# Optimization experiments

Hardware: AMD Instinct MI355X
Metric: run time of the kernel (lower is better)

## Reference

```python
import jax, jax.numpy as jnp
import numpy as np

N_NODES = 50000
N_EDGES = 800000
IN_F = 128
HID = 16
HEADS = 8
OUT_F = 128


def setup_inputs() -> dict:
    key = jax.random.key(0)
    ks = jax.random.split(key, 16)
    h = jax.random.normal(ks[0], (N_NODES, IN_F), dtype=jnp.float32)
    src1 = jax.random.randint(ks[1], (N_EDGES,), 0, N_NODES, dtype=jnp.int32)
    dst1 = jax.random.randint(ks[2], (N_EDGES,), 0, N_NODES, dtype=jnp.int32)
    src2 = jax.random.randint(ks[3], (N_EDGES,), 0, N_NODES, dtype=jnp.int32)
    dst2 = jax.random.randint(ks[4], (N_EDGES,), 0, N_NODES, dtype=jnp.int32)
    norm1 = jax.random.uniform(ks[5], (N_NODES, 1), dtype=jnp.float32)
    norm2 = jax.random.uniform(ks[6], (N_NODES, 1), dtype=jnp.float32)
    D = HEADS * HID  # 128
    W_lin = jax.random.normal(ks[7], (IN_F, D), dtype=jnp.float32) * (1.0 / np.sqrt(IN_F))
    b_lin = jax.random.normal(ks[8], (D,), dtype=jnp.float32) * 0.01
    al = jax.random.normal(ks[9], (HEADS, HID, 1), dtype=jnp.float32) * 0.1
    ar = jax.random.normal(ks[10], (HEADS, HID, 1), dtype=jnp.float32) * 0.1
    W_fc = jax.random.normal(ks[11], (D, OUT_F), dtype=jnp.float32) * (1.0 / np.sqrt(D))
    b_fc = jax.random.normal(ks[12], (OUT_F,), dtype=jnp.float32) * 0.01
    return {"h": h, "src1": src1, "dst1": dst1, "src2": src2, "dst2": dst2,
            "norm1": norm1, "norm2": norm2, "W_lin": W_lin, "b_lin": b_lin,
            "al": al, "ar": ar, "W_fc": W_fc, "b_fc": b_fc}


def _propagate(feat, norm, src, dst, n_nodes):
    # msg = h[src] * norm[src]; accum[v] = sum_{e: dst=v} msg_e; out = accum * norm
    msg = feat[src] * norm[src]                      # [E, D]
    agg = jax.ops.segment_sum(msg, dst, num_segments=n_nodes)
    return agg * norm                                # [N, D]


def _leaky_relu(x):
    return jnp.where(x > 0, x, 0.2 * x)


def reference(h, src1, dst1, src2, dst2, norm1, norm2, W_lin, b_lin, al, ar, W_fc, b_fc):
    N = h.shape[0]
    hf = h @ W_lin + b_lin                           # [N, 8*HID] (dropout p given but eval-mode -> identity)
    h1 = _propagate(hf, norm1, src1, dst1, N)
    h2 = _propagate(hf, norm2, src2, dst2, N)
    # Faithful to torch: row-major reshape [N, 8*HID] -> (8, N, HID)
    h1r = h1.reshape(HEADS, N, HID)
    h2r = h2.reshape(HEADS, N, HID)
    hr = hf.reshape(HEADS, N, HID)
    ai = jnp.einsum('hnd,hdo->hno', hr, al)          # [8, N, 1]
    aj1 = jnp.einsum('hnd,hdo->hno', h1r, ar)
    aj2 = jnp.einsum('hnd,hdo->hno', h2r, ar)
    a1 = jnp.clip(jnp.exp(_leaky_relu(ai + aj1)), -10.0, 10.0)
    a2 = jnp.clip(jnp.exp(_leaky_relu(ai + aj2)), -10.0, 10.0)
    denom = a1 + a2
    out = (a1 / denom) * h1r + (a2 / denom) * h2r    # [8, N, HID]
    out = out.reshape(N, HEADS * HID)
    return out @ W_fc + b_fc
```

## Files before the change

### kernel.cpp

```cpp
#include <hip/hip_runtime.h>

#define NN 50000
#define NE 800000
#define NB 196
#define NBG 392
#define NBLK 128
#define CHUNK 6250
#define MAXB 6144

typedef __bf16 bf16x8 __attribute__((ext_vector_type(8)));
typedef float  f32x4  __attribute__((ext_vector_type(4)));

__device__ __forceinline__ unsigned short f2bf(float x) {
    unsigned u = __float_as_uint(x);
    return (unsigned short)((u + 0x7FFFu + ((u >> 16) & 1u)) >> 16);
}
__device__ __forceinline__ float bflo(unsigned u) { return __uint_as_float(u << 16); }
__device__ __forceinline__ float bfhi(unsigned u) { return __uint_as_float(u & 0xFFFF0000u); }

__global__ __launch_bounds__(1024) void histA_kernel(
    const int* __restrict__ dst1, const int* __restrict__ dst2, int* __restrict__ histG,
    const float* __restrict__ Wa, const float* __restrict__ Wb,
    unsigned short* __restrict__ Wta, unsigned short* __restrict__ Wtb)
{
    const int t = threadIdx.x, blk = blockIdx.x;
    if (blk >= NBLK) {
        const float* W = (blk - NBLK) ? Wb : Wa;
        unsigned short* Wt = (blk - NBLK) ? Wtb : Wta;
        for (int j = t; j < 128 * 128; j += 1024) {
            int n = j >> 7, k = j & 127;
            Wt[j] = f2bf(W[k * 128 + n]);
        }
        return;
    }
    __shared__ int h[NBG];
    for (int i = t; i < NBG; i += 1024) h[i] = 0;
    __syncthreads();
    const int base = blk * CHUNK;
    for (int i = t; i < CHUNK; i += 1024) {
        atomicAdd(&h[dst1[base + i] >> 8], 1);
        atomicAdd(&h[NB + (dst2[base + i] >> 8)], 1);
    }
    __syncthreads();
    for (int i = t; i < NBG; i += 1024)
        histG[blk * NBG + i] = h[i];
}

__global__ __launch_bounds__(1024) void scatterC_kernel(
    const int* __restrict__ src1, const int* __restrict__ dst1,
    const int* __restrict__ src2, const int* __restrict__ dst2,
    const int* __restrict__ histG,
    int* __restrict__ gbbase, int* __restrict__ gbtot,
    unsigned int* __restrict__ bin1, unsigned int* __restrict__ bin2)
{
    __shared__ int s[512];
    __shared__ int pos[NBG];
    const int t = threadIdx.x, blk = blockIdx.x;

    int total_i = 0, pref_i = 0;
    if (t < NBG) {
        for (int c = 0; c < NBLK; c++) {
            int v = histG[c * NBG + t];
            total_i += v;
            if (c < blk) pref_i += v;
        }
    }
    if (t < 512) s[t] = (t < NBG) ? total_i : 0;
    __syncthreads();
    for (int off = 1; off < 512; off <<= 1) {
        int x = 0;
        if (t < 512 && t >= off) x = s[t - off];
        __syncthreads();
        if (t < 512) s[t] += x;
        __syncthreads();
    }
    const int sumG1 = s[NB - 1];
    if (t < NBG) {
        int excl = s[t] - total_i;
        int bb = excl - ((t >= NB) ? sumG1 : 0);
        pos[t] = bb + pref_i;
        if (blk == 0) { gbbase[t] = bb; gbtot[t] = total_i; }
    }
    __syncthreads();

    const int base = blk * CHUNK;
    for (int i = t; i < CHUNK; i += 1024) {
        int d = dst1[base + i], sv = src1[base + i];
        int slot = atomicAdd(&pos[d >> 8], 1);
        bin1[slot] = ((unsigned)(d & 255) << 16) | (unsigned)sv;
        d = dst2[base + i]; sv = src2[base + i];
        slot = atomicAdd(&pos[NB + (d >> 8)], 1);
        bin2[slot] = ((unsigned)(d & 255) << 16) | (unsigned)sv;
    }
}

__global__ __launch_bounds__(256) void bucket_sort_kernel(
    const unsigned int* __restrict__ bin1, const unsigned int* __restrict__ bin2,
    const int* __restrict__ bbase, const int* __restrict__ btot,
    unsigned short* __restrict__ csr1, int* __restrict__ start1, int* __restrict__ deg1,
    unsigned short* __restrict__ csr2, int* __restrict__ start2, int* __restrict__ deg2)
{
    __shared__ int lcnt[256];
    __shared__ int sc[256];
    __shared__ int oat[256];
    __shared__ unsigned short outb[MAXB];
    const int t = threadIdx.x;
    const int g = (blockIdx.x >= NB) ? 1 : 0;
    const int b = blockIdx.x - g * NB;
    const unsigned int* bin = g ? bin2 : bin1;
    unsigned short* csr = g ? csr2 : csr1;
    int* start = g ? start2 : start1;
    int* deg   = g ? deg2 : deg1;

    const int base = bbase[g * NB + b];
    const int tot = min(btot[g * NB + b], MAXB);

    lcnt[t] = 0;
    __syncthreads();
    for (int i = t; i < tot; i += 256) atomicAdd(&lcnt[bin[base + i] >> 16], 1);
    __syncthreads();
    sc[t] = lcnt[t];
    __syncthreads();
    for (int off = 1; off < 256; off <<= 1) {
        int x = (t >= off) ? sc[t - off] : 0;
        __syncthreads();
        sc[t] += x;
        __syncthreads();
    }
    const int ex = sc[t] - lcnt[t];
    oat[t] = ex;
    __syncthreads();
    for (int i = t; i < tot; i += 256) {
        unsigned v = bin[base + i];
        int slot = atomicAdd(&oat[v >> 16], 1);
        outb[slot] = (unsigned short)(v & 0xFFFFu);
    }
    __syncthreads();
    for (int i = t; i < tot; i += 256) csr[base + i] = outb[i];
    int nd = b * 256 + t;
    if (nd < NN) { start[nd] = base + ex; deg[nd] = lcnt[t]; }
}

__global__ __launch_bounds__(256) void mfma_gemm_kernel(
    const float* __restrict__ X, const unsigned short* __restrict__ Wt,
    const float* __restrict__ bias, float* __restrict__ Y,
    unsigned short* __restrict__ Ybf, int nrows)
{
    __shared__ unsigned short Wl[128 * 128];
    const int t = threadIdx.x;
    const int lane = t & 63;
    const int wv = t >> 6;
    const int row0 = blockIdx.x * 64;
    const int m16 = lane & 15;
    const int quad = lane >> 4;

    {
        const uint4* Wg = (const uint4*)Wt;
        #pragma unroll
        for (int i = 0; i < 8; i++) {
            int gi = t + i * 256;
            int n = gi >> 4, g = gi & 15;
            uint4 v = Wg[gi];
            *(uint4*)&Wl[n * 128 + (((g ^ (n & 15)) << 3))] = v;
        }
    }

    const int arow = row0 + wv * 16 + m16;
    const bool valid = (arow < nrows);
    const float4* X4 = (const float4*)X;
    float4 xr[8];
    #pragma unroll
    for (int kc = 0; kc < 4; kc++) {
        if (valid) {
            int gidx = arow * 32 + kc * 8 + quad * 2;
            xr[kc * 2]     = X4[gidx];
            xr[kc * 2 + 1] = X4[gidx + 1];
        } else {
            xr[kc * 2] = xr[kc * 2 + 1] = make_float4(0.f, 0.f, 0.f, 0.f);
        }
    }
    __syncthreads();

    f32x4 acc[8];
    #pragma unroll
    for (int nt = 0; nt < 8; nt++) acc[nt] = (f32x4){0.f, 0.f, 0.f, 0.f};

    #pragma unroll
    for (int kc = 0; kc < 4; kc++) {
        union { unsigned short u[8]; bf16x8 v; } ah, al;
        float f[8] = { xr[kc*2].x, xr[kc*2].y, xr[kc*2].z, xr[kc*2].w,
                       xr[kc*2+1].x, xr[kc*2+1].y, xr[kc*2+1].z, xr[kc*2+1].w };
        #pragma unroll
        for (int j = 0; j < 8; j++) {
            unsigned u = __float_as_uint(f[j]);
            ah.u[j] = (unsigned short)(u >> 16);
            al.u[j] = f2bf(f[j] - __uint_as_float(u & 0xFFFF0000u));
        }
        const int sgbase = (kc * 4 + quad);
        #pragma unroll
        for (int nt = 0; nt < 8; nt++) {
            const int n = nt * 16 + m16;
            bf16x8 b = *(const bf16x8*)&Wl[n * 128 + ((sgbase ^ m16) << 3)];
            acc[nt] = __builtin_amdgcn_mfma_f32_16x16x32_bf16(ah.v, b, acc[nt], 0, 0, 0);
            acc[nt] = __builtin_amdgcn_mfma_f32_16x16x32_bf16(al.v, b, acc[nt], 0, 0, 0);
        }
    }

    #pragma unroll
    for (int nt = 0; nt < 8; nt++) {
        const int col = nt * 16 + m16;
        const float bc = bias[col];
        #pragma unroll
        for (int r = 0; r < 4; r++) {
            int row = row0 + wv * 16 + quad * 4 + r;
            if (row < nrows) {
                float val = acc[nt][r] + bc;
                if (Y)   Y[(long)row * 128 + col] = val;
                if (Ybf) Ybf[(long)row * 128 + col] = f2bf(val);
            }
        }
    }
}

__global__ __launch_bounds__(256) void mfma_gemm_bf16_kernel(
    const unsigned short* __restrict__ Xbf, const unsigned short* __restrict__ Wt,
    const float* __restrict__ bias, float* __restrict__ Y, int nrows)
{
    __shared__ unsigned short Wl[128 * 128];
    const int t = threadIdx.x;
    const int lane = t & 63;
    const int wv = t >> 6;
    const int row0 = blockIdx.x * 64;
    const int m16 = lane & 15;
    const int quad = lane >> 4;

    {
        const uint4* Wg = (const uint4*)Wt;
        #pragma unroll
        for (int i = 0; i < 8; i++) {
            int gi = t + i * 256;
            int n = gi >> 4, g = gi & 15;
            uint4 v = Wg[gi];
            *(uint4*)&Wl[n * 128 + (((g ^ (n & 15)) << 3))] = v;
        }
    }

    const int arow = row0 + wv * 16 + m16;
    const bool valid = (arow < nrows);
    const uint4* X16 = (const uint4*)Xbf;
    union { uint4 u; bf16x8 v; } xr[4];
    #pragma unroll
    for (int kc = 0; kc < 4; kc++) {
        if (valid) xr[kc].u = X16[arow * 16 + kc * 4 + quad];
        else       xr[kc].u = make_uint4(0, 0, 0, 0);
    }
    __syncthreads();

    f32x4 acc[8];
    #pragma unroll
    for (int nt = 0; nt < 8; nt++) acc[nt] = (f32x4){0.f, 0.f, 0.f, 0.f};

    #pragma unroll
    for (int kc = 0; kc < 4; kc++) {
        const int sgbase = (kc * 4 + quad);
        #pragma unroll
        for (int nt = 0; nt < 8; nt++) {
            const int n = nt * 16 + m16;
            bf16x8 b = *(const bf16x8*)&Wl[n * 128 + ((sgbase ^ m16) << 3)];
            acc[nt] = __builtin_amdgcn_mfma_f32_16x16x32_bf16(xr[kc].v, b, acc[nt], 0, 0, 0);
        }
    }

    #pragma unroll
    for (int nt = 0; nt < 8; nt++) {
        const int col = nt * 16 + m16;
        const float bc = bias[col];
        #pragma unroll
        for (int r = 0; r < 4; r++) {
            int row = row0 + wv * 16 + quad * 4 + r;
            if (row < nrows) Y[(long)row * 128 + col] = acc[nt][r] + bc;
        }
    }
}

__global__ __launch_bounds__(256) void gather_attn_kernel(
    const unsigned int* __restrict__ hfb,
    const unsigned short* __restrict__ csr1, const int* __restrict__ start1,
    const int* __restrict__ deg1, const float* __restrict__ norm1,
    const unsigned short* __restrict__ csr2, const int* __restrict__ start2,
    const int* __restrict__ deg2, const float* __restrict__ norm2,
    const float* __restrict__ al, const float* __restrict__ ar,
    unsigned int* __restrict__ outb)
{
    const int lane = threadIdx.x & 63;
    int node = (blockIdx.x * 256 + threadIdx.x) >> 6;
    if (node >= NN) return;
    node = __builtin_amdgcn_readfirstlane(node);

    float2 acc1 = make_float2(0.f, 0.f), acc2 = make_float2(0.f, 0.f);

    #pragma unroll 1
    for (int g = 0; g < 2; g++) {
        const unsigned short* csr = g ? csr2 : csr1;
        const int* startp = g ? start2 : start1;
        const int* degp   = g ? deg2 : deg1;
        const float* norm = g ? norm2 : norm1;
        float2 acc = make_float2(0.f, 0.f);
        const int st = startp[node], dg = degp[node];
        for (int base = 0; base < dg; base += 64) {
            const int nb = min(64, dg - base);
            int myc = (lane < nb) ? (int)csr[st + base + lane] : 0;
            int j = 0;
            for (; j + 8 <= nb; j += 8) {
                int s[8]; float n[8]; unsigned u[8];
                #pragma unroll
                for (int q = 0; q < 8; q++) s[q] = __builtin_amdgcn_readlane(myc, j + q);
                #pragma unroll
                for (int q = 0; q < 8; q++) {
                    n[q] = norm[s[q]];
                    u[q] = hfb[(long)s[q] * 64 + lane];
                }
                #pragma unroll
                for (int q = 0; q < 8; q++) {
                    acc.x = fmaf(bflo(u[q]), n[q], acc.x);
                    acc.y = fmaf(bfhi(u[q]), n[q], acc.y);
                }
            }
            for (; j < nb; j++) {
                int s = __builtin_amdgcn_readlane(myc, j);
                float nv = norm[s];
                unsigned u = hfb[(long)s * 64 + lane];
                acc.x = fmaf(bflo(u), nv, acc.x);
                acc.y = fmaf(bfhi(u), nv, acc.y);
            }
        }
        if (g) acc2 = acc; else acc1 = acc;
    }

    const float nn1 = norm1[node], nn2 = norm2[node];
    acc1.x *= nn1; acc1.y *= nn1;
    acc2.x *= nn2; acc2.y *= nn2;

    const int cc = lane >> 3;
    const int m = node * 8 + cc;
    const int head = m / NN;
    const int hid = (2 * lane) & 15;
    unsigned uf = hfb[(long)node * 64 + lane];
    const float fx = bflo(uf), fy = bfhi(uf);
    const float av0 = al[head * 16 + hid], av1 = al[head * 16 + hid + 1];
    const float rv0 = ar[head * 16 + hid], rv1 = ar[head * 16 + hid + 1];
    float s_ai = fx * av0 + fy * av1;
    float s1 = acc1.x * rv0 + acc1.y * rv1;
    float s2 = acc2.x * rv0 + acc2.y * rv1;
    s_ai += __shfl_xor(s_ai, 1); s_ai += __shfl_xor(s_ai, 2); s_ai += __shfl_xor(s_ai, 4);
    s1   += __shfl_xor(s1, 1);   s1   += __shfl_xor(s1, 2);   s1   += __shfl_xor(s1, 4);
    s2   += __shfl_xor(s2, 1);   s2   += __shfl_xor(s2, 2);   s2   += __shfl_xor(s2, 4);
    float x1 = s_ai + s1; x1 = x1 > 0.f ? x1 : 0.2f * x1;
    float x2 = s_ai + s2; x2 = x2 > 0.f ? x2 : 0.2f * x2;
    float e1 = fminf(expf(x1), 10.f);
    float e2 = fminf(expf(x2), 10.f);
    float inv = 1.f / (e1 + e2);
    float w1 = e1 * inv, w2 = e2 * inv;
    float ox = w1 * acc1.x + w2 * acc2.x;
    float oy = w1 * acc1.y + w2 * acc2.y;
    outb[(long)node * 64 + lane] = (unsigned)f2bf(ox) | ((unsigned)f2bf(oy) << 16);
}

extern "C" void kernel_launch(void* const* d_in, const int* in_sizes, int n_in,
                              void* d_out, int out_size, void* d_ws, size_t ws_size,
                              hipStream_t stream)
{
    const float* h     = (const float*)d_in[0];
    const int*   src1  = (const int*)  d_in[1];
    const int*   dst1  = (const int*)  d_in[2];
    const int*   src2  = (const int*)  d_in[3];
    const int*   dst2  = (const int*)  d_in[4];
    const float* norm1 = (const float*)d_in[5];
    const float* norm2 = (const float*)d_in[6];
    const float* W_lin = (const float*)d_in[7];
    const float* b_lin = (const float*)d_in[8];
    const float* al    = (const float*)d_in[9];
    const float* ar    = (const float*)d_in[10];
    const float* W_fc  = (const float*)d_in[11];
    const float* b_fc  = (const float*)d_in[12];
    float* out = (float*)d_out;

    unsigned short* hfb  = (unsigned short*)d_ws;
    unsigned short* outbf = hfb + (size_t)NN * 128;
    unsigned int* bin1 = (unsigned int*)(outbf + (size_t)NN * 128);
    unsigned int* bin2 = bin1 + NE;
    unsigned short* csr1 = (unsigned short*)(bin2 + NE);
    unsigned short* csr2 = csr1 + NE;
    unsigned short* WtL  = csr2 + NE;
    unsigned short* WtF  = WtL + 128 * 128;
    int* histG  = (int*)(WtF + 128 * 128);
    int* btot   = histG + NBLK * NBG;
    int* bbase  = btot + NBG;
    int* start1 = bbase + NBG;
    int* start2 = start1 + NN;
    int* deg1   = start2 + NN;
    int* deg2   = deg1 + NN;

    histA_kernel<<<NBLK + 2, 1024, 0, stream>>>(dst1, dst2, histG, W_lin, W_fc, WtL, WtF);

    mfma_gemm_kernel<<<(NN + 63) / 64, 256, 0, stream>>>(h, WtL, b_lin, nullptr, hfb, NN);

    scatterC_kernel<<<NBLK, 1024, 0, stream>>>(src1, dst1, src2, dst2, histG,
                                               bbase, btot, bin1, bin2);

    bucket_sort_kernel<<<NBG, 256, 0, stream>>>(bin1, bin2, bbase, btot,
                                                csr1, start1, deg1,
                                                csr2, start2, deg2);

    gather_attn_kernel<<<(NN * 64) / 256, 256, 0, stream>>>(
        (const unsigned int*)hfb,
        csr1, start1, deg1, norm1,
        csr2, start2, deg2, norm2,
        al, ar, (unsigned int*)outbf);

    mfma_gemm_bf16_kernel<<<(NN + 63) / 64, 256, 0, stream>>>(outbf, WtF, b_fc, out, NN);
}
```

Baseline: 229.8 us.

## Pre-scale features by norms in GEMM and batch neighbor gathers for both graphs

The first GEMM now also writes two bf16 copies of the features pre-multiplied by norm1 and norm2. This removes the per-edge norm gather and the multiply from the aggregation kernel. The gather kernel then issues up to 32 neighbor loads per graph into registers before summing, so memory parallelism is higher, and it falls back to a scalar loop for high-degree nodes. The cost is two extra N×128 bf16 writes and much higher register pressure from the 64 unrolled load slots, which may reduce occupancy. Pre-scaling also rounds the product to bf16, which changes numerics slightly.

```diff
diff --git a/kernel.cpp b/kernel.cpp
--- a/kernel.cpp
+++ b/kernel.cpp
@@ -143,8 +143,10 @@
 
 __global__ __launch_bounds__(256) void mfma_gemm_kernel(
     const float* __restrict__ X, const unsigned short* __restrict__ Wt,
-    const float* __restrict__ bias, float* __restrict__ Y,
-    unsigned short* __restrict__ Ybf, int nrows)
+    const float* __restrict__ bias,
+    const float* __restrict__ norm1, const float* __restrict__ norm2,
+    unsigned short* __restrict__ Ybf, unsigned short* __restrict__ Y1,
+    unsigned short* __restrict__ Y2, int nrows)
 {
     __shared__ unsigned short Wl[128 * 128];
     const int t = threadIdx.x;
@@ -179,6 +181,14 @@
             xr[kc * 2] = xr[kc * 2 + 1] = make_float4(0.f, 0.f, 0.f, 0.f);
         }
     }
+
+    float n1c[4], n2c[4];
+    #pragma unroll
+    for (int r = 0; r < 4; r++) {
+        int row = row0 + wv * 16 + quad * 4 + r;
+        if (row < nrows) { n1c[r] = norm1[row]; n2c[r] = norm2[row]; }
+        else             { n1c[r] = 0.f;        n2c[r] = 0.f; }
+    }
     __syncthreads();
 
     f32x4 acc[8];
@@ -215,8 +225,9 @@
             int row = row0 + wv * 16 + quad * 4 + r;
             if (row < nrows) {
                 float val = acc[nt][r] + bc;
-                if (Y)   Y[(long)row * 128 + col] = val;
-                if (Ybf) Ybf[(long)row * 128 + col] = f2bf(val);
+                Ybf[(long)row * 128 + col] = f2bf(val);
+                Y1[(long)row * 128 + col] = f2bf(val * n1c[r]);
+                Y2[(long)row * 128 + col] = f2bf(val * n2c[r]);
             }
         }
     }
@@ -285,6 +296,8 @@
 
 __global__ __launch_bounds__(256) void gather_attn_kernel(
     const unsigned int* __restrict__ hfb,
+    const unsigned int* __restrict__ hfb1,
+    const unsigned int* __restrict__ hfb2,
     const unsigned short* __restrict__ csr1, const int* __restrict__ start1,
     const int* __restrict__ deg1, const float* __restrict__ norm1,
     const unsigned short* __restrict__ csr2, const int* __restrict__ start2,
@@ -297,44 +310,51 @@
     if (node >= NN) return;
     node = __builtin_amdgcn_readfirstlane(node);
 
+    const unsigned uf = hfb[(long)node * 64 + lane];
+
+    const int st1 = start1[node], dg1 = deg1[node];
+    const int st2 = start2[node], dg2 = deg2[node];
+    const int nb1 = (dg1 < 32) ? dg1 : 32;
+    const int nb2 = (dg2 < 32) ? dg2 : 32;
+
+    int myc1 = (lane < nb1) ? (int)csr1[st1 + lane] : 0;
+    int myc2 = (lane < nb2) ? (int)csr2[st2 + lane] : 0;
+
+    unsigned uA[32], uB[32];
+    #pragma unroll
+    for (int q = 0; q < 32; q++) {
+        if (q < nb1) {
+            int s = __builtin_amdgcn_readlane(myc1, q);
+            uA[q] = hfb1[((long)s << 6) + lane];
+        }
+    }
+    #pragma unroll
+    for (int q = 0; q < 32; q++) {
+        if (q < nb2) {
+            int s = __builtin_amdgcn_readlane(myc2, q);
+            uB[q] = hfb2[((long)s << 6) + lane];
+        }
+    }
+
     float2 acc1 = make_float2(0.f, 0.f), acc2 = make_float2(0.f, 0.f);
-
-    #pragma unroll 1
-    for (int g = 0; g < 2; g++) {
-        const unsigned short* csr = g ? csr2 : csr1;
-        const int* startp = g ? start2 : start1;
-        const int* degp   = g ? deg2 : deg1;
-        const float* norm = g ? norm2 : norm1;
-        float2 acc = make_float2(0.f, 0.f);
-        const int st = startp[node], dg = degp[node];
-        for (int base = 0; base < dg; base += 64) {
-            const int nb = min(64, dg - base);
-            int myc = (lane < nb) ? (int)csr[st + base + lane] : 0;
-            int j = 0;
-            for (; j + 8 <= nb; j += 8) {
-                int s[8]; float n[8]; unsigned u[8];
-                #pragma unroll
-                for (int q = 0; q < 8; q++) s[q] = __builtin_amdgcn_readlane(myc, j + q);
-                #pragma unroll
-                for (int q = 0; q < 8; q++) {
-                    n[q] = norm[s[q]];
-                    u[q] = hfb[(long)s[q] * 64 + lane];
-                }
-                #pragma unroll
-                for (int q = 0; q < 8; q++) {
-                    acc.x = fmaf(bflo(u[q]), n[q], acc.x);
-                    acc.y = fmaf(bfhi(u[q]), n[q], acc.y);
-                }
-            }
-            for (; j < nb; j++) {
-                int s = __builtin_amdgcn_readlane(myc, j);
-                float nv = norm[s];
-                unsigned u = hfb[(long)s * 64 + lane];
-                acc.x = fmaf(bflo(u), nv, acc.x);
-                acc.y = fmaf(bfhi(u), nv, acc.y);
-            }
-        }
-        if (g) acc2 = acc; else acc1 = acc;
+    #pragma unroll
+    for (int q = 0; q < 32; q++) {
+        if (q < nb1) { acc1.x += bflo(uA[q]); acc1.y += bfhi(uA[q]); }
+    }
+    #pragma unroll
+    for (int q = 0; q < 32; q++) {
+        if (q < nb2) { acc2.x += bflo(uB[q]); acc2.y += bfhi(uB[q]); }
+    }
+
+    for (int e = 32; e < dg1; e++) {
+        int s = (int)csr1[st1 + e];
+        unsigned u = hfb1[((long)s << 6) + lane];
+        acc1.x += bflo(u); acc1.y += bfhi(u);
+    }
+    for (int e = 32; e < dg2; e++) {
+        int s = (int)csr2[st2 + e];
+        unsigned u = hfb2[((long)s << 6) + lane];
+        acc2.x += bflo(u); acc2.y += bfhi(u);
     }
 
     const float nn1 = norm1[node], nn2 = norm2[node];
@@ -345,7 +365,6 @@
     const int m = node * 8 + cc;
     const int head = m / NN;
     const int hid = (2 * lane) & 15;
-    unsigned uf = hfb[(long)node * 64 + lane];
     const float fx = bflo(uf), fy = bfhi(uf);
     const float av0 = al[head * 16 + hid], av1 = al[head * 16 + hid + 1];
     const float rv0 = ar[head * 16 + hid], rv1 = ar[head * 16 + hid + 1];
@@ -400,10 +419,13 @@
     int* start2 = start1 + NN;
     int* deg1   = start2 + NN;
     int* deg2   = deg1 + NN;
+    unsigned short* hfb1 = (unsigned short*)(deg2 + NN);
+    unsigned short* hfb2 = hfb1 + (size_t)NN * 128;
 
     histA_kernel<<<NBLK + 2, 1024, 0, stream>>>(dst1, dst2, histG, W_lin, W_fc, WtL, WtF);
 
-    mfma_gemm_kernel<<<(NN + 63) / 64, 256, 0, stream>>>(h, WtL, b_lin, nullptr, hfb, NN);
+    mfma_gemm_kernel<<<(NN + 63) / 64, 256, 0, stream>>>(h, WtL, b_lin, norm1, norm2,
+                                                         hfb, hfb1, hfb2, NN);
 
     scatterC_kernel<<<NBLK, 1024, 0, stream>>>(src1, dst1, src2, dst2, histG,
                                                bbase, btot, bin1, bin2);
@@ -413,7 +435,7 @@
                                                 csr2, start2, deg2);
 
     gather_attn_kernel<<<(NN * 64) / 256, 256, 0, stream>>>(
-        (const unsigned int*)hfb,
+        (const unsigned int*)hfb, (const unsigned int*)hfb1, (const unsigned int*)hfb2,
         csr1, start1, deg1, norm1,
         csr2, start2, deg2, norm2,
         al, ar, (unsigned int*)outbf);
```

Result: slower. 262.5 us (+14.3%).

## Issue all neighbor row loads via global_load_lds into LDS before accumulating

Applied to the files above, without the earlier changes.

The gather kernel now issues up to 32 neighbor feature-row loads per graph straight into LDS with global_load_lds, waits once, and then accumulates from LDS. Neighbor norms are loaded per lane and broadcast with readlane, and any neighbors beyond 32 fall back to a serial global loop. The goal is more memory requests in flight per wave, hiding gather latency instead of exposing it in groups of eight. In exchange it uses 32KB of LDS per 128-thread block, which may limit occupancy, and blocks shrink to two waves.

```diff
diff --git a/kernel.cpp b/kernel.cpp
--- a/kernel.cpp
+++ b/kernel.cpp
@@ -17,6 +17,15 @@
 }
 __device__ __forceinline__ float bflo(unsigned u) { return __uint_as_float(u << 16); }
 __device__ __forceinline__ float bfhi(unsigned u) { return __uint_as_float(u & 0xFFFF0000u); }
+
+__device__ __forceinline__ void gload_lds(const unsigned* g, unsigned* l) {
+    __builtin_amdgcn_global_load_lds(
+        (const __attribute__((address_space(1))) unsigned*)g,
+        (__attribute__((address_space(3))) unsigned*)l, 4, 0, 0);
+}
+__device__ __forceinline__ float readlane_f(float v, int q) {
+    return __uint_as_float(__builtin_amdgcn_readlane(__float_as_uint(v), q));
+}
 
 __global__ __launch_bounds__(1024) void histA_kernel(
     const int* __restrict__ dst1, const int* __restrict__ dst2, int* __restrict__ histG,
@@ -283,7 +292,7 @@
     }
 }
 
-__global__ __launch_bounds__(256) void gather_attn_kernel(
+__global__ __launch_bounds__(128) void gather_attn_kernel(
     const unsigned int* __restrict__ hfb,
     const unsigned short* __restrict__ csr1, const int* __restrict__ start1,
     const int* __restrict__ deg1, const float* __restrict__ norm1,
@@ -292,49 +301,82 @@
     const float* __restrict__ al, const float* __restrict__ ar,
     unsigned int* __restrict__ outb)
 {
+    __shared__ unsigned stage[2 * 64 * 64];
     const int lane = threadIdx.x & 63;
-    int node = (blockIdx.x * 256 + threadIdx.x) >> 6;
+    int node = (blockIdx.x * 128 + threadIdx.x) >> 6;
     if (node >= NN) return;
     node = __builtin_amdgcn_readfirstlane(node);
+    unsigned* mybuf = stage + ((threadIdx.x >> 6) << 12);
+
+    const unsigned uf = hfb[(long)node * 64 + lane];
+
+    const int st1 = start1[node], dg1 = deg1[node];
+    const int st2 = start2[node], dg2 = deg2[node];
+    const int nb1 = (dg1 < 32) ? dg1 : 32;
+    const int nb2 = (dg2 < 32) ? dg2 : 32;
+
+    int myc1 = (lane < nb1) ? (int)csr1[st1 + lane] : 0;
+    int myc2 = (lane < nb2) ? (int)csr2[st2 + lane] : 0;
+    const float nv1 = norm1[myc1];
+    const float nv2 = norm2[myc2];
+
+    #pragma unroll
+    for (int g8 = 0; g8 < 4; g8++) {
+        if (g8 * 8 < nb1) {
+            #pragma unroll
+            for (int k = 0; k < 8; k++) {
+                int q = g8 * 8 + k;
+                int qq = (q < nb1) ? q : (nb1 - 1);
+                int s = __builtin_amdgcn_readlane(myc1, qq);
+                gload_lds(&hfb[(long)s * 64 + lane], &mybuf[q * 64]);
+            }
+        }
+    }
+    #pragma unroll
+    for (int g8 = 0; g8 < 4; g8++) {
+        if (g8 * 8 < nb2) {
+            #pragma unroll
+            for (int k = 0; k < 8; k++) {
+                int q = g8 * 8 + k;
+                int qq = (q < nb2) ? q : (nb2 - 1);
+                int s = __builtin_amdgcn_readlane(myc2, qq);
+                gload_lds(&hfb[(long)s * 64 + lane], &mybuf[(32 + q) * 64]);
+            }
+        }
+    }
+
+    asm volatile("s_waitcnt vmcnt(0)" ::: "memory");
+    __builtin_amdgcn_sched_barrier(0);
 
     float2 acc1 = make_float2(0.f, 0.f), acc2 = make_float2(0.f, 0.f);
-
-    #pragma unroll 1
-    for (int g = 0; g < 2; g++) {
-        const unsigned short* csr = g ? csr2 : csr1;
-        const int* startp = g ? start2 : start1;
-        const int* degp   = g ? deg2 : deg1;
-        const float* norm = g ? norm2 : norm1;
-        float2 acc = make_float2(0.f, 0.f);
-        const int st = startp[node], dg = degp[node];
-        for (int base = 0; base < dg; base += 64) {
-            const int nb = min(64, dg - base);
-            int myc = (lane < nb) ? (int)csr[st + base + lane] : 0;
-            int j = 0;
-            for (; j + 8 <= nb; j += 8) {
-                int s[8]; float n[8]; unsigned u[8];
-                #pragma unroll
-                for (int q = 0; q < 8; q++) s[q] = __builtin_amdgcn_readlane(myc, j + q);
-                #pragma unroll
-                for (int q = 0; q < 8; q++) {
-                    n[q] = norm[s[q]];
-                    u[q] = hfb[(long)s[q] * 64 + lane];
-                }
-                #pragma unroll
-                for (int q = 0; q < 8; q++) {
-                    acc.x = fmaf(bflo(u[q]), n[q], acc.x);
-                    acc.y = fmaf(bfhi(u[q]), n[q], acc.y);
-                }
-            }
-            for (; j < nb; j++) {
-                int s = __builtin_amdgcn_readlane(myc, j);
-                float nv = norm[s];
-                unsigned u = hfb[(long)s * 64 + lane];
-                acc.x = fmaf(bflo(u), nv, acc.x);
-                acc.y = fmaf(bfhi(u), nv, acc.y);
-            }
-        }
-        if (g) acc2 = acc; else acc1 = acc;
+    #pragma unroll 4
+    for (int q = 0; q < nb1; q++) {
+        unsigned u = mybuf[q * 64 + lane];
+        float n = readlane_f(nv1, q);
+        acc1.x = fmaf(bflo(u), n, acc1.x);
+        acc1.y = fmaf(bfhi(u), n, acc1.y);
+    }
+    #pragma unroll 4
+    for (int q = 0; q < nb2; q++) {
+        unsigned u = mybuf[(32 + q) * 64 + lane];
+        float n = readlane_f(nv2, q);
+        acc2.x = fmaf(bflo(u), n, acc2.x);
+        acc2.y = fmaf(bfhi(u), n, acc2.y);
+    }
+
+    for (int e = 32; e < dg1; e++) {
+        int s = (int)csr1[st1 + e];
+        float n = norm1[s];
+        unsigned u = hfb[(long)s * 64 + lane];
+        acc1.x = fmaf(bflo(u), n, acc1.x);
+        acc1.y = fmaf(bfhi(u), n, acc1.y);
+    }
+    for (int e = 32; e < dg2; e++) {
+        int s = (int)csr2[st2 + e];
+        float n = norm2[s];
+        unsigned u = hfb[(long)s * 64 + lane];
+        acc2.x = fmaf(bflo(u), n, acc2.x);
+        acc2.y = fmaf(bfhi(u), n, acc2.y);
     }
 
     const float nn1 = norm1[node], nn2 = norm2[node];
@@ -345,7 +387,6 @@
     const int m = node * 8 + cc;
     const int head = m / NN;
     const int hid = (2 * lane) & 15;
-    unsigned uf = hfb[(long)node * 64 + lane];
     const float fx = bflo(uf), fy = bfhi(uf);
     const float av0 = al[head * 16 + hid], av1 = al[head * 16 + hid + 1];
     const float rv0 = ar[head * 16 + hid], rv1 = ar[head * 16 + hid + 1];
@@ -412,7 +453,7 @@
                                                 csr1, start1, deg1,
                                                 csr2, start2, deg2);
 
-    gather_attn_kernel<<<(NN * 64) / 256, 256, 0, stream>>>(
+    gather_attn_kernel<<<(NN + 1) / 2, 128, 0, stream>>>(
         (const unsigned int*)hfb,
         csr1, start1, deg1, norm1,
         csr2, start2, deg2, norm2,
```

After: 289.2 us. 25.9% more time.

## Split bf16 feature table into column halves for cache-friendlier gather

Applied to the files above, without the earlier changes.

The first GEMM now writes the projected features as two separate bf16 tables, one per 64-column half, each 128 bytes per row. The gather-attention kernel launches twice as many wavefronts: each handles one node and one column half, and interleaves half assignments across blocks so concurrently running blocks read the same half-table. This shrinks the working set of the random gathers so they fit better in cache, but the CSR indices and norms are read twice, loads become 16-bit, and the per-head reduction needs one more shuffle step.

```diff
diff --git a/kernel.cpp b/kernel.cpp
--- a/kernel.cpp
+++ b/kernel.cpp
@@ -15,8 +15,9 @@
     unsigned u = __float_as_uint(x);
     return (unsigned short)((u + 0x7FFFu + ((u >> 16) & 1u)) >> 16);
 }
-__device__ __forceinline__ float bflo(unsigned u) { return __uint_as_float(u << 16); }
-__device__ __forceinline__ float bfhi(unsigned u) { return __uint_as_float(u & 0xFFFF0000u); }
+__device__ __forceinline__ float bf2f(unsigned short u) {
+    return __uint_as_float(((unsigned)u) << 16);
+}
 
 __global__ __launch_bounds__(1024) void histA_kernel(
     const int* __restrict__ dst1, const int* __restrict__ dst2, int* __restrict__ histG,
@@ -143,8 +144,8 @@
 
 __global__ __launch_bounds__(256) void mfma_gemm_kernel(
     const float* __restrict__ X, const unsigned short* __restrict__ Wt,
-    const float* __restrict__ bias, float* __restrict__ Y,
-    unsigned short* __restrict__ Ybf, int nrows)
+    const float* __restrict__ bias,
+    unsigned short* __restrict__ YA, unsigned short* __restrict__ YB, int nrows)
 {
     __shared__ unsigned short Wl[128 * 128];
     const int t = threadIdx.x;
@@ -215,8 +216,8 @@
             int row = row0 + wv * 16 + quad * 4 + r;
             if (row < nrows) {
                 float val = acc[nt][r] + bc;
-                if (Y)   Y[(long)row * 128 + col] = val;
-                if (Ybf) Ybf[(long)row * 128 + col] = f2bf(val);
+                if (col < 64) YA[(long)row * 64 + col]        = f2bf(val);
+                else          YB[(long)row * 64 + (col - 64)] = f2bf(val);
             }
         }
     }
@@ -284,20 +285,26 @@
 }
 
 __global__ __launch_bounds__(256) void gather_attn_kernel(
-    const unsigned int* __restrict__ hfb,
+    const unsigned short* __restrict__ hfA, const unsigned short* __restrict__ hfB,
     const unsigned short* __restrict__ csr1, const int* __restrict__ start1,
     const int* __restrict__ deg1, const float* __restrict__ norm1,
     const unsigned short* __restrict__ csr2, const int* __restrict__ start2,
     const int* __restrict__ deg2, const float* __restrict__ norm2,
     const float* __restrict__ al, const float* __restrict__ ar,
-    unsigned int* __restrict__ outb)
+    unsigned short* __restrict__ outb)
 {
     const int lane = threadIdx.x & 63;
-    int node = (blockIdx.x * 256 + threadIdx.x) >> 6;
-    if (node >= NN) return;
+    const int wv = threadIdx.x >> 6;
+    const int b = blockIdx.x;
+    const int half = (b >> 2) & 1;
+    const int lb = (b >> 3) * 4 + (b & 3);
+    int node = lb * 4 + wv;
     node = __builtin_amdgcn_readfirstlane(node);
-
-    float2 acc1 = make_float2(0.f, 0.f), acc2 = make_float2(0.f, 0.f);
+    const unsigned short* tbl = half ? hfB : hfA;
+
+    const float uf = bf2f(tbl[(long)node * 64 + lane]);
+
+    float acc1 = 0.f, acc2 = 0.f;
 
     #pragma unroll 1
     for (int g = 0; g < 2; g++) {
@@ -305,65 +312,63 @@
         const int* startp = g ? start2 : start1;
         const int* degp   = g ? deg2 : deg1;
         const float* norm = g ? norm2 : norm1;
-        float2 acc = make_float2(0.f, 0.f);
+        float acc = 0.f;
         const int st = startp[node], dg = degp[node];
         for (int base = 0; base < dg; base += 64) {
             const int nb = min(64, dg - base);
             int myc = (lane < nb) ? (int)csr[st + base + lane] : 0;
             int j = 0;
             for (; j + 8 <= nb; j += 8) {
-                int s[8]; float n[8]; unsigned u[8];
+                int s[8]; float n[8]; unsigned short u[8];
                 #pragma unroll
                 for (int q = 0; q < 8; q++) s[q] = __builtin_amdgcn_readlane(myc, j + q);
                 #pragma unroll
                 for (int q = 0; q < 8; q++) {
                     n[q] = norm[s[q]];
-                    u[q] = hfb[(long)s[q] * 64 + lane];
+                    u[q] = tbl[(long)s[q] * 64 + lane];
                 }
                 #pragma unroll
-                for (int q = 0; q < 8; q++) {
-                    acc.x = fmaf(bflo(u[q]), n[q], acc.x);
-                    acc.y = fmaf(bfhi(u[q]), n[q], acc.y);
-                }
+                for (int q = 0; q < 8; q++)
+                    acc = fmaf(bf2f(u[q]), n[q], acc);
             }
             for (; j < nb; j++) {
                 int s = __builtin_amdgcn_readlane(myc, j);
                 float nv = norm[s];
-                unsigned u = hfb[(long)s * 64 + lane];
-                acc.x = fmaf(bflo(u), nv, acc.x);
-                acc.y = fmaf(bfhi(u), nv, acc.y);
+                unsigned short u = tbl[(long)s * 64 + lane];
+                acc = fmaf(bf2f(u), nv, acc);
             }
         }
         if (g) acc2 = acc; else acc1 = acc;
     }
 
     const float nn1 = norm1[node], nn2 = norm2[node];
-    acc1.x *= nn1; acc1.y *= nn1;
-    acc2.x *= nn2; acc2.y *= nn2;
-
-    const int cc = lane >> 3;
+    acc1 *= nn1;
+    acc2 *= nn2;
+
+    const int c = half * 64 + lane;
+    const int cc = c >> 4;
     const int m = node * 8 + cc;
     const int head = m / NN;
-    const int hid = (2 * lane) & 15;
-    unsigned uf = hfb[(long)node * 64 + lane];
-    const float fx = bflo(uf), fy = bfhi(uf);
-    const float av0 = al[head * 16 + hid], av1 = al[head * 16 + hid + 1];
-    const float rv0 = ar[head * 16 + hid], rv1 = ar[head * 16 + hid + 1];
-    float s_ai = fx * av0 + fy * av1;
-    float s1 = acc1.x * rv0 + acc1.y * rv1;
-    float s2 = acc2.x * rv0 + acc2.y * rv1;
-    s_ai += __shfl_xor(s_ai, 1); s_ai += __shfl_xor(s_ai, 2); s_ai += __shfl_xor(s_ai, 4);
-    s1   += __shfl_xor(s1, 1);   s1   += __shfl_xor(s1, 2);   s1   += __shfl_xor(s1, 4);
-    s2   += __shfl_xor(s2, 1);   s2   += __shfl_xor(s2, 2);   s2   += __shfl_xor(s2, 4);
+    const int hid = c & 15;
+    const float av = al[head * 16 + hid];
+    const float rv = ar[head * 16 + hid];
+    float s_ai = uf * av;
+    float s1 = acc1 * rv;
+    float s2 = acc2 * rv;
+    s_ai += __shfl_xor(s_ai, 1); s_ai += __shfl_xor(s_ai, 2);
+    s_ai += __shfl_xor(s_ai, 4); s_ai += __shfl_xor(s_ai, 8);
+    s1   += __shfl_xor(s1, 1);   s1   += __shfl_xor(s1, 2);
+    s1   += __shfl_xor(s1, 4);   s1   += __shfl_xor(s1, 8);
+    s2   += __shfl_xor(s2, 1);   s2   += __shfl_xor(s2, 2);
+    s2   += __shfl_xor(s2, 4);   s2   += __shfl_xor(s2, 8);
     float x1 = s_ai + s1; x1 = x1 > 0.f ? x1 : 0.2f * x1;
     float x2 = s_ai + s2; x2 = x2 > 0.f ? x2 : 0.2f * x2;
     float e1 = fminf(expf(x1), 10.f);
     float e2 = fminf(expf(x2), 10.f);
     float inv = 1.f / (e1 + e2);
     float w1 = e1 * inv, w2 = e2 * inv;
-    float ox = w1 * acc1.x + w2 * acc2.x;
-    float oy = w1 * acc1.y + w2 * acc2.y;
-    outb[(long)node * 64 + lane] = (unsigned)f2bf(ox) | ((unsigned)f2bf(oy) << 16);
+    float o = w1 * acc1 + w2 * acc2;
+    outb[(long)node * 128 + c] = f2bf(o);
 }
 
 extern "C" void kernel_launch(void* const* d_in, const int* in_sizes, int n_in,
@@ -385,8 +390,9 @@
     const float* b_fc  = (const float*)d_in[12];
     float* out = (float*)d_out;
 
-    unsigned short* hfb  = (unsigned short*)d_ws;
-    unsigned short* outbf = hfb + (size_t)NN * 128;
+    unsigned short* hfA  = (unsigned short*)d_ws;
+    unsigned short* hfB  = hfA + (size_t)NN * 64;
+    unsigned short* outbf = hfB + (size_t)NN * 64;
     unsigned int* bin1 = (unsigned int*)(outbf + (size_t)NN * 128);
     unsigned int* bin2 = bin1 + NE;
     unsigned short* csr1 = (unsigned short*)(bin2 + NE);
@@ -403,7 +409,7 @@
 
     histA_kernel<<<NBLK + 2, 1024, 0, stream>>>(dst1, dst2, histG, W_lin, W_fc, WtL, WtF);
 
-    mfma_gemm_kernel<<<(NN + 63) / 64, 256, 0, stream>>>(h, WtL, b_lin, nullptr, hfb, NN);
+    mfma_gemm_kernel<<<(NN + 63) / 64, 256, 0, stream>>>(h, WtL, b_lin, hfA, hfB, NN);
 
     scatterC_kernel<<<NBLK, 1024, 0, stream>>>(src1, dst1, src2, dst2, histG,
                                                bbase, btot, bin1, bin2);
@@ -412,11 +418,11 @@
                                                 csr1, start1, deg1,
                                                 csr2, start2, deg2);
 
-    gather_attn_kernel<<<(NN * 64) / 256, 256, 0, stream>>>(
-        (const unsigned int*)hfb,
+    gather_attn_kernel<<<25000, 256, 0, stream>>>(
+        hfA, hfB,
         csr1, start1, deg1, norm1,
         csr2, start2, deg2, norm2,
-        al, ar, (unsigned int*)outbf);
+        al, ar, outbf);
 
     mfma_gemm_bf16_kernel<<<(NN + 63) / 64, 256, 0, stream>>>(outbf, WtF, b_fc, out, NN);
 }
```

Result: slower. 260.2 us (+13.2%).
